# Performance work log

Hardware: AMD Instinct MI355X
Metric: run time of the kernel (lower is better)

Reference implementation:

```python
import jax, jax.numpy as jnp
import numpy as np


def setup_inputs() -> dict:
    key = jax.random.key(0)
    k1, k2, k3, k4 = jax.random.split(key, 4)
    B, Sq, Sk, d = 16, 2048, 2048, 64
    queries = jax.random.normal(k1, (B, Sq, d), dtype=jnp.float32)
    keys = jax.random.normal(k2, (B, Sk, d), dtype=jnp.float32)
    values = jax.random.normal(k3, (B, Sk, d), dtype=jnp.float32)
    # True = padded key position (masked out)
    key_padding_mask = jax.random.randint(k4, (B, Sk), 0, 2) == 1
    return {"queries": queries, "keys": keys, "values": values,
            "key_padding_mask": key_padding_mask}


def reference(queries, keys, values, key_padding_mask):
    d = queries.shape[-1]
    # scores: [B, Sq, Sk]
    scores = jnp.einsum("bqd,bkd->bqk", queries, keys) / jnp.sqrt(
        jnp.asarray(d, dtype=queries.dtype))
    # padded keys get -inf before softmax (mask broadcast over query dim)
    scores = jnp.where(key_padding_mask[:, None, :], -jnp.inf, scores)
    attention_weights = jax.nn.softmax(scores, axis=2)
    return jnp.einsum("bqk,bkd->bqd", attention_weights, values)
```

## Files before the change

kernel.cpp:

```cpp
#include <hip/hip_runtime.h>
#include <hip/hip_bf16.h>

#define NB 16
#define SQ 2048
#define SK 2048
#define DH 64

#define KBLK 1024
#define VBLK 512
#define BBLK 128

typedef __attribute__((ext_vector_type(8))) short short8;
typedef __attribute__((ext_vector_type(8))) __bf16 bf16x8;
typedef __attribute__((ext_vector_type(4))) float floatx4;
typedef __attribute__((ext_vector_type(16))) float floatx16;
typedef __attribute__((ext_vector_type(2))) unsigned uint2v;

#define GLOB const __attribute__((address_space(1))) void*
#define LDSP __attribute__((address_space(3))) void*

__device__ __forceinline__ unsigned pk2(float a, float b) {
  __hip_bfloat162 h = __float22bfloat162_rn(make_float2(a, b));
  unsigned u; __builtin_memcpy(&u, &h, 4); return u;
}
__device__ __forceinline__ floatx16 mfma32(short8 a, short8 b, floatx16 c) {
  return __builtin_amdgcn_mfma_f32_32x32x16_bf16(
      __builtin_bit_cast(bf16x8, a), __builtin_bit_cast(bf16x8, b), c, 0, 0, 0);
}

__device__ __forceinline__ int swap23(int k) {
  return (((k >> 2) ^ (k >> 3)) & 1) ? (k ^ 12) : k;
}

__global__ __launch_bounds__(256)
void prepass(const float* __restrict__ K, const float* __restrict__ V,
             const int* __restrict__ m, short* __restrict__ Kb,
             short* __restrict__ Vt, float* __restrict__ bias) {
  __shared__ unsigned tlw[64 * 33];
  const int blk = blockIdx.x;
  const int t = threadIdx.x;
  if (blk < KBLK) {
    size_t i8 = ((size_t)blk * 256 + t) * 8;
    floatx4 a = *(const floatx4*)(K + i8);
    floatx4 b = *(const floatx4*)(K + i8 + 4);
    union { unsigned u[4]; short8 s; } w;
    w.u[0] = pk2(a[0], a[1]); w.u[1] = pk2(a[2], a[3]);
    w.u[2] = pk2(b[0], b[1]); w.u[3] = pk2(b[2], b[3]);
    const int local = (int)(i8 & 4095);
    const int key = local >> 6, chunk = (local >> 3) & 7;
    const int prow = swap23(key);
    const size_t tb = i8 & ~(size_t)4095;
    *(short8*)(Kb + tb + prow * 64 + ((chunk ^ (prow & 7)) << 3)) = w.s;
  } else if (blk < KBLK + VBLK) {
    const int bt = blk - KBLK;
    const int key2 = t & 31;
    const int dg = (t >> 5) * 8;
    const float* vp0 = V + ((size_t)bt * 64 + 2 * key2) * 64 + dg;
    const float* vp1 = vp0 + 64;
    floatx4 va  = *(const floatx4*)(vp0);
    floatx4 va2 = *(const floatx4*)(vp0 + 4);
    floatx4 vb  = *(const floatx4*)(vp1);
    floatx4 vb2 = *(const floatx4*)(vp1 + 4);
#pragma unroll
    for (int j = 0; j < 4; ++j) {
      tlw[(dg + j) * 33 + key2]     = pk2(va[j],  vb[j]);
      tlw[(dg + 4 + j) * 33 + key2] = pk2(va2[j], vb2[j]);
    }
    __syncthreads();
    const short* tls = (const short*)tlw;
    short* dst = Vt + (size_t)bt * 4096;
#pragma unroll
    for (int i = 0; i < 2; ++i) {
      int idx = i * 2048 + t * 8;
      int d = idx >> 6, key = idx & 63;
      int chunk = key >> 3;
      *(short8*)(dst + d * 64 + ((chunk ^ (d & 7)) << 3)) =
          *(const short8*)(tls + d * 66 + key);
    }
  } else {
    int i = (blk - KBLK - VBLK) * 256 + t;
    bias[i] = m[i] ? -1e30f : 0.0f;
  }
}

__global__ __launch_bounds__(256, 4)
void attn_main(const float* __restrict__ Q, const short* __restrict__ Kb,
               const short* __restrict__ Vt, const float* __restrict__ bias,
               float* __restrict__ Out, float* __restrict__ Op,
               float* __restrict__ lsum) {
  __shared__ __align__(16) short ks[2][4096];
  __shared__ __align__(16) short vt[2][4096];
  __shared__ __align__(16) float bsh[512];

  const int gid = blockIdx.x;
  const int xcd = gid & 7;
  const int j   = gid >> 3;
  const int cmb = xcd + 8 * (j >> 4);
  const int part = cmb >> 4;
  const int b    = cmb & 15;
  const int qt   = j & 15;
  const int tid  = threadIdx.x;
  const int wave = tid >> 6;
  const int lane = tid & 63;
  const int n32  = lane & 31;
  const int h    = lane >> 5;
  const int sw   = n32 & 7;
  const int q0   = qt * 128 + wave * 32;
  const int kt0  = part << 3;

  const float QS = 0.125f * 1.4426950408889634f;
  short8 qf[4];
  {
    const float* qp = Q + ((size_t)b * SQ + q0 + n32) * DH + 8 * h;
#pragma unroll
    for (int c = 0; c < 4; ++c) {
      floatx4 a  = *(const floatx4*)(qp + 16 * c);
      floatx4 a2 = *(const floatx4*)(qp + 16 * c + 4);
      union { unsigned u[4]; short8 s; } w;
      w.u[0] = pk2(a[0] * QS, a[1] * QS);
      w.u[1] = pk2(a[2] * QS, a[3] * QS);
      w.u[2] = pk2(a2[0] * QS, a2[1] * QS);
      w.u[3] = pk2(a2[2] * QS, a2[3] * QS);
      qf[c] = w.s;
    }
  }

  if (tid < 128) {
    floatx4 bv = *(const floatx4*)(bias + (size_t)b * SK + kt0 * 64 + tid * 4);
    *(floatx4*)(bsh + tid * 4) = bv;
  }

  floatx16 o0, o1;
#pragma unroll
  for (int i = 0; i < 16; ++i) { o0[i] = 0.f; o1[i] = 0.f; }
  float l_q = 0.f;

  const short* kg = Kb + (size_t)b * SK * DH;
  const short* vg = Vt + (size_t)b * 32 * 4096;

  const int lo0 = (wave * 2) * 512;
  const int lo1 = (wave * 2 + 1) * 512;
  const int go0 = lo0 + lane * 8;
  const int go1 = lo1 + lane * 8;

  {
    const short* kn = kg + (size_t)kt0 * 4096;
    const short* vn = vg + (size_t)kt0 * 4096;
    __builtin_amdgcn_global_load_lds((GLOB)(kn + go0), (LDSP)&ks[0][lo0], 16, 0, 0);
    __builtin_amdgcn_global_load_lds((GLOB)(kn + go1), (LDSP)&ks[0][lo1], 16, 0, 0);
    __builtin_amdgcn_global_load_lds((GLOB)(vn + go0), (LDSP)&vt[0][lo0], 16, 0, 0);
    __builtin_amdgcn_global_load_lds((GLOB)(vn + go1), (LDSP)&vt[0][lo1], 16, 0, 0);
  }
  __syncthreads();

  int p = 0;
  for (int it = 0; it < 8; ++it) {
    if (it + 1 < 8) {
      const int kt = kt0 + it;
      const short* kn = kg + (size_t)(kt + 1) * 4096;
      const short* vn = vg + (size_t)(kt + 1) * 4096;
      __builtin_amdgcn_global_load_lds((GLOB)(kn + go0), (LDSP)&ks[p ^ 1][lo0], 16, 0, 0);
      __builtin_amdgcn_global_load_lds((GLOB)(kn + go1), (LDSP)&ks[p ^ 1][lo1], 16, 0, 0);
      __builtin_amdgcn_global_load_lds((GLOB)(vn + go0), (LDSP)&vt[p ^ 1][lo0], 16, 0, 0);
      __builtin_amdgcn_global_load_lds((GLOB)(vn + go1), (LDSP)&vt[p ^ 1][lo1], 16, 0, 0);
    }

    const float* bq = bsh + it * 64 + 8 * h;
    floatx16 s0, s1;
#pragma unroll
    for (int u = 0; u < 4; ++u) {
      const int off = 16 * (u >> 1) + 4 * (u & 1);
      floatx4 bv0 = *(const floatx4*)(bq + off);
      floatx4 bv1 = *(const floatx4*)(bq + 32 + off);
#pragma unroll
      for (int i = 0; i < 4; ++i) { s0[4 * u + i] = bv0[i]; s1[4 * u + i] = bv1[i]; }
    }
#pragma unroll
    for (int c = 0; c < 4; ++c) {
      short8 kf0 = *(short8*)(ks[p] + n32 * 64        + ((2 * c + h) ^ sw) * 8);
      short8 kf1 = *(short8*)(ks[p] + (32 + n32) * 64 + ((2 * c + h) ^ sw) * 8);
      s0 = mfma32(kf0, qf[c], s0);
      s1 = mfma32(kf1, qf[c], s1);
    }

    uint2v pka[4], pkb[4];
    float rs = 0.f;
#pragma unroll
    for (int u = 0; u < 4; ++u) {
      float p0 = __builtin_amdgcn_exp2f(s0[4 * u + 0]);
      float p1 = __builtin_amdgcn_exp2f(s0[4 * u + 1]);
      float p2 = __builtin_amdgcn_exp2f(s0[4 * u + 2]);
      float p3 = __builtin_amdgcn_exp2f(s0[4 * u + 3]);
      float r0 = __builtin_amdgcn_exp2f(s1[4 * u + 0]);
      float r1 = __builtin_amdgcn_exp2f(s1[4 * u + 1]);
      float r2 = __builtin_amdgcn_exp2f(s1[4 * u + 2]);
      float r3 = __builtin_amdgcn_exp2f(s1[4 * u + 3]);
      rs += ((p0 + p1) + (p2 + p3)) + ((r0 + r1) + (r2 + r3));
      pka[u].x = pk2(p0, p1); pka[u].y = pk2(p2, p3);
      pkb[u].x = pk2(r0, r1); pkb[u].y = pk2(r2, r3);
    }
    l_q += rs;

#pragma unroll
    for (int c = 0; c < 4; ++c) {
      const uint2v* X = (c < 2) ? pka : pkb;
      union { unsigned u[4]; short8 s; } pf;
      pf.u[0] = X[2 * (c & 1)].x;     pf.u[1] = X[2 * (c & 1)].y;
      pf.u[2] = X[2 * (c & 1) + 1].x; pf.u[3] = X[2 * (c & 1) + 1].y;
      short8 vf0 = *(short8*)(vt[p] + n32 * 64        + ((2 * c + h) ^ sw) * 8);
      short8 vf1 = *(short8*)(vt[p] + (32 + n32) * 64 + ((2 * c + h) ^ sw) * 8);
      o0 = mfma32(vf0, pf.s, o0);
      o1 = mfma32(vf1, pf.s, o1);
    }
    __syncthreads();
    p ^= 1;
  }

  l_q += __shfl_xor(l_q, 32);

  float* Od = part ? (Op + (size_t)(part - 1) * NB * SQ * DH) : Out;
  float* orow = Od + ((size_t)b * SQ + q0 + n32) * DH;
#pragma unroll
  for (int u = 0; u < 4; ++u) {
    floatx4 w0, w1;
#pragma unroll
    for (int i = 0; i < 4; ++i) { w0[i] = o0[4 * u + i]; w1[i] = o1[4 * u + i]; }
    *(floatx4*)(orow + 8 * u + 4 * h)      = w0;
    *(floatx4*)(orow + 32 + 8 * u + 4 * h) = w1;
  }
  if (lane < 32)
    lsum[(size_t)part * NB * SQ + (size_t)b * SQ + q0 + lane] = l_q;
}

__global__ __launch_bounds__(256)
void combine(const float* __restrict__ Op, const float* __restrict__ lsum,
             float* __restrict__ Out) {
  int idx = blockIdx.x * 256 + threadIdx.x;
  int q = idx >> 3;
  int dc = (idx & 7) * 8;
  float inv = 1.0f / (lsum[q] + lsum[NB * SQ + q] +
                      lsum[2 * NB * SQ + q] + lsum[3 * NB * SQ + q]);
  const size_t base = (size_t)q * DH + dc;
  const size_t stride = (size_t)NB * SQ * DH;
  floatx4 a0 = *(const floatx4*)(Out + base);
  floatx4 a1 = *(const floatx4*)(Out + base + 4);
  floatx4 b0 = *(const floatx4*)(Op + base);
  floatx4 b1 = *(const floatx4*)(Op + base + 4);
  floatx4 c0 = *(const floatx4*)(Op + stride + base);
  floatx4 c1 = *(const floatx4*)(Op + stride + base + 4);
  floatx4 d0 = *(const floatx4*)(Op + 2 * stride + base);
  floatx4 d1 = *(const floatx4*)(Op + 2 * stride + base + 4);
  *(floatx4*)(Out + base)     = (a0 + b0 + c0 + d0) * inv;
  *(floatx4*)(Out + base + 4) = (a1 + b1 + c1 + d1) * inv;
}

extern "C" void kernel_launch(void* const* d_in, const int* in_sizes, int n_in,
                              void* d_out, int out_size, void* d_ws, size_t ws_size,
                              hipStream_t stream) {
  const float* Q = (const float*)d_in[0];
  const float* K = (const float*)d_in[1];
  const float* V = (const float*)d_in[2];
  const int* mask = (const int*)d_in[3];
  float* Out = (float*)d_out;

  char* ws = (char*)d_ws;
  short* Kb   = (short*)(ws);
  short* Vt   = (short*)(ws + 4194304);
  float* bias = (float*)(ws + 8388608);
  float* lsum = (float*)(ws + 8519680);
  float* Op   = (float*)(ws + 9043968);

  prepass  <<<KBLK + VBLK + BBLK, 256, 0, stream>>>(K, V, mask, Kb, Vt, bias);
  attn_main<<<4 * NB * (SQ / 128), 256, 0, stream>>>(Q, Kb, Vt, bias, Out, Op, lsum);
  combine  <<<NB * SQ * DH / 8 / 256, 256, 0, stream>>>(Op, lsum, Out);
}
```

Measured before the change: 110.3 us.

## Software-pipeline QK of next tile with softmax and PV of current tile

Restructures the attention loop so the QK MFMA for tile t+1 is issued while the exp/pack and PV MFMAs for tile t run, using double-buffered score registers. K and V tile loads are now issued separately, two tiles ahead, and gated with explicit s_waitcnt vmcnt counts and raw s_barrier instead of __syncthreads. The aim is to hide LDS load latency and the MFMA-to-exp dependency, and to give the copies more time to land. The cost is higher register pressure from the extra score accumulators, and correctness now depends on hand-counted vmcnt values.

```diff
diff --git a/kernel.cpp b/kernel.cpp
--- a/kernel.cpp
+++ b/kernel.cpp
@@ -135,71 +135,79 @@
   for (int i = 0; i < 16; ++i) { o0[i] = 0.f; o1[i] = 0.f; }
   float l_q = 0.f;
 
-  const short* kg = Kb + (size_t)b * SK * DH;
-  const short* vg = Vt + (size_t)b * 32 * 4096;
+  const short* kg = Kb + ((size_t)b * SK + (size_t)kt0 * 64) * DH;
+  const short* vg = Vt + ((size_t)b * 32 + kt0) * 4096;
 
   const int lo0 = (wave * 2) * 512;
   const int lo1 = (wave * 2 + 1) * 512;
   const int go0 = lo0 + lane * 8;
   const int go1 = lo1 + lane * 8;
 
-  {
-    const short* kn = kg + (size_t)kt0 * 4096;
-    const short* vn = vg + (size_t)kt0 * 4096;
-    __builtin_amdgcn_global_load_lds((GLOB)(kn + go0), (LDSP)&ks[0][lo0], 16, 0, 0);
-    __builtin_amdgcn_global_load_lds((GLOB)(kn + go1), (LDSP)&ks[0][lo1], 16, 0, 0);
-    __builtin_amdgcn_global_load_lds((GLOB)(vn + go0), (LDSP)&vt[0][lo0], 16, 0, 0);
-    __builtin_amdgcn_global_load_lds((GLOB)(vn + go1), (LDSP)&vt[0][lo1], 16, 0, 0);
-  }
-  __syncthreads();
-
-  int p = 0;
-  for (int it = 0; it < 8; ++it) {
-    if (it + 1 < 8) {
-      const int kt = kt0 + it;
-      const short* kn = kg + (size_t)(kt + 1) * 4096;
-      const short* vn = vg + (size_t)(kt + 1) * 4096;
-      __builtin_amdgcn_global_load_lds((GLOB)(kn + go0), (LDSP)&ks[p ^ 1][lo0], 16, 0, 0);
-      __builtin_amdgcn_global_load_lds((GLOB)(kn + go1), (LDSP)&ks[p ^ 1][lo1], 16, 0, 0);
-      __builtin_amdgcn_global_load_lds((GLOB)(vn + go0), (LDSP)&vt[p ^ 1][lo0], 16, 0, 0);
-      __builtin_amdgcn_global_load_lds((GLOB)(vn + go1), (LDSP)&vt[p ^ 1][lo1], 16, 0, 0);
-    }
-
-    const float* bq = bsh + it * 64 + 8 * h;
-    floatx16 s0, s1;
-#pragma unroll
-    for (int u = 0; u < 4; ++u) {
-      const int off = 16 * (u >> 1) + 4 * (u & 1);
-      floatx4 bv0 = *(const floatx4*)(bq + off);
-      floatx4 bv1 = *(const floatx4*)(bq + 32 + off);
-#pragma unroll
-      for (int i = 0; i < 4; ++i) { s0[4 * u + i] = bv0[i]; s1[4 * u + i] = bv1[i]; }
-    }
-#pragma unroll
-    for (int c = 0; c < 4; ++c) {
-      short8 kf0 = *(short8*)(ks[p] + n32 * 64        + ((2 * c + h) ^ sw) * 8);
-      short8 kf1 = *(short8*)(ks[p] + (32 + n32) * 64 + ((2 * c + h) ^ sw) * 8);
-      s0 = mfma32(kf0, qf[c], s0);
-      s1 = mfma32(kf1, qf[c], s1);
-    }
+#define ISSUE_K(tile, buf) do {                                                        \
+    const short* kn_ = kg + (size_t)(tile) * 4096;                                     \
+    __builtin_amdgcn_global_load_lds((GLOB)(kn_ + go0), (LDSP)&ks[buf][lo0], 16, 0, 0);\
+    __builtin_amdgcn_global_load_lds((GLOB)(kn_ + go1), (LDSP)&ks[buf][lo1], 16, 0, 0);\
+  } while (0)
+#define ISSUE_V(tile, buf) do {                                                        \
+    const short* vn_ = vg + (size_t)(tile) * 4096;                                     \
+    __builtin_amdgcn_global_load_lds((GLOB)(vn_ + go0), (LDSP)&vt[buf][lo0], 16, 0, 0);\
+    __builtin_amdgcn_global_load_lds((GLOB)(vn_ + go1), (LDSP)&vt[buf][lo1], 16, 0, 0);\
+  } while (0)
+
+  floatx16 sA[2], sB[2];
+
+#define QK(tt, d) do {                                                                 \
+    const float* bq_ = bsh + (tt) * 64 + 8 * h;                                        \
+    _Pragma("unroll") for (int u = 0; u < 4; ++u) {                                    \
+      const int off_ = 16 * (u >> 1) + 4 * (u & 1);                                    \
+      floatx4 bv0_ = *(const floatx4*)(bq_ + off_);                                    \
+      floatx4 bv1_ = *(const floatx4*)(bq_ + 32 + off_);                               \
+      _Pragma("unroll") for (int i = 0; i < 4; ++i) {                                  \
+        sA[d][4 * u + i] = bv0_[i]; sB[d][4 * u + i] = bv1_[i]; } }                    \
+    _Pragma("unroll") for (int c = 0; c < 4; ++c) {                                    \
+      short8 kf0_ = *(short8*)(ks[(tt) & 1] + n32 * 64        + ((2 * c + h) ^ sw) * 8);\
+      short8 kf1_ = *(short8*)(ks[(tt) & 1] + (32 + n32) * 64 + ((2 * c + h) ^ sw) * 8);\
+      sA[d] = mfma32(kf0_, qf[c], sA[d]);                                              \
+      sB[d] = mfma32(kf1_, qf[c], sB[d]); }                                            \
+  } while (0)
+
+  asm volatile("s_waitcnt vmcnt(0) lgkmcnt(0)" ::: "memory");
+  __builtin_amdgcn_sched_barrier(0);
+  ISSUE_K(0, 0); ISSUE_V(0, 0); ISSUE_K(1, 1); ISSUE_V(1, 1);
+  asm volatile("s_waitcnt vmcnt(6)" ::: "memory");
+  __builtin_amdgcn_s_barrier();
+  __builtin_amdgcn_sched_barrier(0);
+  QK(0, 0);
+
+#pragma unroll
+  for (int t = 0; t < 8; ++t) {
+    if (t < 7) asm volatile("s_waitcnt vmcnt(2)" ::: "memory");
+    else       asm volatile("s_waitcnt vmcnt(0)" ::: "memory");
+    __builtin_amdgcn_s_barrier();
+    __builtin_amdgcn_sched_barrier(0);
+
+    if (t < 6) ISSUE_K(t + 2, t & 1);
 
     uint2v pka[4], pkb[4];
-    float rs = 0.f;
-#pragma unroll
-    for (int u = 0; u < 4; ++u) {
-      float p0 = __builtin_amdgcn_exp2f(s0[4 * u + 0]);
-      float p1 = __builtin_amdgcn_exp2f(s0[4 * u + 1]);
-      float p2 = __builtin_amdgcn_exp2f(s0[4 * u + 2]);
-      float p3 = __builtin_amdgcn_exp2f(s0[4 * u + 3]);
-      float r0 = __builtin_amdgcn_exp2f(s1[4 * u + 0]);
-      float r1 = __builtin_amdgcn_exp2f(s1[4 * u + 1]);
-      float r2 = __builtin_amdgcn_exp2f(s1[4 * u + 2]);
-      float r3 = __builtin_amdgcn_exp2f(s1[4 * u + 3]);
-      rs += ((p0 + p1) + (p2 + p3)) + ((r0 + r1) + (r2 + r3));
-      pka[u].x = pk2(p0, p1); pka[u].y = pk2(p2, p3);
-      pkb[u].x = pk2(r0, r1); pkb[u].y = pk2(r2, r3);
-    }
-    l_q += rs;
+    {
+      float rs = 0.f;
+#pragma unroll
+      for (int u = 0; u < 4; ++u) {
+        float p0 = __builtin_amdgcn_exp2f(sA[t & 1][4 * u + 0]);
+        float p1 = __builtin_amdgcn_exp2f(sA[t & 1][4 * u + 1]);
+        float p2 = __builtin_amdgcn_exp2f(sA[t & 1][4 * u + 2]);
+        float p3 = __builtin_amdgcn_exp2f(sA[t & 1][4 * u + 3]);
+        float r0 = __builtin_amdgcn_exp2f(sB[t & 1][4 * u + 0]);
+        float r1 = __builtin_amdgcn_exp2f(sB[t & 1][4 * u + 1]);
+        float r2 = __builtin_amdgcn_exp2f(sB[t & 1][4 * u + 2]);
+        float r3 = __builtin_amdgcn_exp2f(sB[t & 1][4 * u + 3]);
+        rs += ((p0 + p1) + (p2 + p3)) + ((r0 + r1) + (r2 + r3));
+        pka[u].x = pk2(p0, p1); pka[u].y = pk2(p2, p3);
+        pkb[u].x = pk2(r0, r1); pkb[u].y = pk2(r2, r3);
+      }
+      l_q += rs;
+    }
+    if (t < 7) QK(t + 1, (t + 1) & 1);
 
 #pragma unroll
     for (int c = 0; c < 4; ++c) {
@@ -207,14 +215,21 @@
       union { unsigned u[4]; short8 s; } pf;
       pf.u[0] = X[2 * (c & 1)].x;     pf.u[1] = X[2 * (c & 1)].y;
       pf.u[2] = X[2 * (c & 1) + 1].x; pf.u[3] = X[2 * (c & 1) + 1].y;
-      short8 vf0 = *(short8*)(vt[p] + n32 * 64        + ((2 * c + h) ^ sw) * 8);
-      short8 vf1 = *(short8*)(vt[p] + (32 + n32) * 64 + ((2 * c + h) ^ sw) * 8);
+      short8 vf0 = *(short8*)(vt[t & 1] + n32 * 64        + ((2 * c + h) ^ sw) * 8);
+      short8 vf1 = *(short8*)(vt[t & 1] + (32 + n32) * 64 + ((2 * c + h) ^ sw) * 8);
       o0 = mfma32(vf0, pf.s, o0);
       o1 = mfma32(vf1, pf.s, o1);
     }
-    __syncthreads();
-    p ^= 1;
-  }
+
+    if (t < 6) {
+      __builtin_amdgcn_s_barrier();
+      __builtin_amdgcn_sched_barrier(0);
+      ISSUE_V(t + 2, t & 1);
+    }
+  }
+#undef ISSUE_K
+#undef ISSUE_V
+#undef QK
 
   l_q += __shfl_xor(l_q, 32);
 
```

Result: no change. 110.9 us (+0.6%).
